# Performance work log

Hardware: AMD Instinct MI355X
Metric: run time of the kernel (lower is better)

The kernel has to match this reference:

```python
import jax, jax.numpy as jnp
import numpy as np

N, IN_DIM, H, ATT_DIM, OUT_DIM = 4096, 512, 8, 64, 64
ATT_BIAS = 0.5


def setup_inputs() -> dict:
    key = jax.random.key(0)
    ks = jax.random.split(key, 12)
    s_in = 1.0 / np.sqrt(IN_DIM)
    s_o = 1.0 / np.sqrt(H * OUT_DIM)
    return {
        "Q": jax.random.normal(ks[0], (N, IN_DIM), jnp.float32),
        "K": jax.random.normal(ks[1], (N, IN_DIM), jnp.float32),
        "V": jax.random.normal(ks[2], (N, IN_DIM), jnp.float32),
        "adj": jax.random.uniform(ks[3], (N, N), jnp.float32),
        "WQ": jax.random.normal(ks[4], (IN_DIM, H * ATT_DIM), jnp.float32) * s_in,
        "bQ": jnp.zeros((H * ATT_DIM,), jnp.float32),
        "WK": jax.random.normal(ks[5], (IN_DIM, H * ATT_DIM), jnp.float32) * s_in,
        "bK": jnp.zeros((H * ATT_DIM,), jnp.float32),
        "WV": jax.random.normal(ks[6], (IN_DIM, H * OUT_DIM), jnp.float32) * s_in,
        "bV": jnp.zeros((H * OUT_DIM,), jnp.float32),
        "WO": jax.random.normal(ks[7], (H * OUT_DIM, OUT_DIM), jnp.float32) * s_o,
        "bO": jnp.zeros((OUT_DIM,), jnp.float32),
    }


def reference(Q, K, V, adj, WQ, bQ, WK, bK, WV, bV, WO, bO):
    scale = ATT_DIM ** -0.5
    q = (Q @ WQ + bQ).reshape(N, H, ATT_DIM)   # [N,H,d]
    k = (K @ WK + bK).reshape(N, H, ATT_DIM)   # [N,H,d]
    v = (V @ WV + bV).reshape(N, H, OUT_DIM)   # [N,H,e]
    # scaled QK^T per head: [H,N,N]
    scores = jnp.einsum("nhd,mhd->hnm", q * scale, k)
    # sigmoid -> bias subtract -> +0.1*adj -> softmax over keys
    scores = jax.nn.sigmoid(scores) - ATT_BIAS + 0.1 * adj[None, :, :]
    attn = jax.nn.softmax(scores, axis=2)
    # attend values (dropout p=0 => identity), concat heads, project
    out = jnp.einsum("hnm,mhe->nhe", attn, v).reshape(N, H * OUT_DIM)
    return out @ WO + bO
```

## Files before the change

kernel.cpp:

```cpp
#include <hip/hip_runtime.h>
#include <hip/hip_bf16.h>

#define N_TOK  4096
#define HD     512
#define NH     8
#define NSPLIT 4
#define QBLK   128
#define NT     ((N_TOK / NSPLIT) / 64)

typedef short v8s __attribute__((ext_vector_type(8)));
typedef float v4f __attribute__((ext_vector_type(4)));
typedef float v16f __attribute__((ext_vector_type(16)));
typedef unsigned short u16;

#define QSCALE   0.18033688011112042f
#define ADJ2     0.14426950408889634f
#define EA0 0.999410f
#define EA1 1.016220f
#define EA2 0.423120f
#define EA3 0.279120f

__device__ __forceinline__ float bf2f(u16 x) {
  union { unsigned int u; float f; } c; c.u = ((unsigned int)x) << 16; return c.f;
}
__device__ __forceinline__ u16 f2bf(float f) {
  union { float f; unsigned int u; } c; c.f = f;
  return (u16)((c.u + 0x7fffu + ((c.u >> 16) & 1u)) >> 16);
}
__device__ __forceinline__ float fast_exp2(float x) {
#if __has_builtin(__builtin_amdgcn_exp2f)
  return __builtin_amdgcn_exp2f(x);
#else
  return exp2f(x);
#endif
}
__device__ __forceinline__ unsigned int pk_bf16(float a, float b) {
  union { __hip_bfloat162 h; unsigned int u; } c;
  c.h = __float22bfloat162_rn(make_float2(a, b));
  return c.u;
}

typedef __attribute__((address_space(1))) const char gchar;
typedef __attribute__((address_space(3))) char lchar;
__device__ __forceinline__ void glds16(const void* g, void* l) {
  __builtin_amdgcn_global_load_lds((gchar*)g, (lchar*)l, 16, 0, 0);
}
__device__ __forceinline__ void plswap(unsigned int& a, unsigned int& b) {
  asm volatile("v_permlane32_swap_b32 %0, %1" : "+v"(a), "+v"(b));
}

__device__ __forceinline__ bool detect_f32(const u16* __restrict__ q) {
  int l = threadIdx.x & 63;
  u16 e = q[2 * l];
  float x = bf2f(e);
  int ex = (e >> 7) & 0xFF;
  float ax = fabsf(x);
  bool ok = (ex != 0xFF) && (ax < 64.f) && (ax > 1e-30f);
  unsigned long long m = __ballot(ok);
  return __popcll(m) < 48;
}
__device__ __forceinline__ float bias_ld(const void* b, int i, bool f32) {
  return f32 ? ((const float*)b)[i] : bf2f(((const u16*)b)[i]);
}

__global__ __launch_bounds__(256) void conv_adjE_k(const void* __restrict__ adj, u16* __restrict__ adjE,
                                                   const u16* __restrict__ Qdet) {
  bool f32 = detect_f32(Qdet);
  int i = blockIdx.x * 256 + threadIdx.x;
  float4 f;
  if (f32) {
    f = ((const float4*)adj)[i];
  } else {
    short4 v = ((const short4*)adj)[i];
    f.x = bf2f((u16)v.x); f.y = bf2f((u16)v.y); f.z = bf2f((u16)v.z); f.w = bf2f((u16)v.w);
  }
  unsigned int d0 = pk_bf16(fast_exp2(f.x * ADJ2), fast_exp2(f.y * ADJ2));
  unsigned int d1 = pk_bf16(fast_exp2(f.z * ADJ2), fast_exp2(f.w * ADJ2));
  ((uint2*)adjE)[i] = make_uint2(d0, d1);
}

__global__ __launch_bounds__(256) void tr_w_k(const void* W0, const void* W1, const void* W2, const void* W3,
                                              u16* t0, u16* t1, u16* t2, u16* t3,
                                              const u16* __restrict__ Qdet) {
  bool f32 = detect_f32(Qdet);
  int z = blockIdx.z;
  const void* in; u16* out; int C;
  if (z == 0)      { in = W0; out = t0; C = 512; }
  else if (z == 1) { in = W1; out = t1; C = 512; }
  else if (z == 2) { in = W2; out = t2; C = 512; }
  else             { in = W3; out = t3; C = 64; if (blockIdx.y) return; }
  const int R = 512;
  __shared__ __align__(16) u16 tile[64][72];
  const int r0 = blockIdx.x * 64, c0 = blockIdx.y * 64;
  const int t = threadIdx.x;
#pragma unroll
  for (int rep = 0; rep < 2; ++rep) {
    int idx = (t + rep * 256) * 8;
    int r = idx >> 6, c = idx & 63;
    if (f32) {
      const float* sp = (const float*)in + (size_t)(r0 + r) * C + (c0 + c);
      float4 a = *(const float4*)sp, b = *(const float4*)(sp + 4);
      uint4 q = make_uint4(pk_bf16(a.x, a.y), pk_bf16(a.z, a.w),
                           pk_bf16(b.x, b.y), pk_bf16(b.z, b.w));
      *(uint4*)&tile[r][c] = q;
    } else {
      *(v8s*)&tile[r][c] = *(const v8s*)((const u16*)in + (size_t)(r0 + r) * C + (c0 + c));
    }
  }
  __syncthreads();
#pragma unroll
  for (int rep = 0; rep < 2; ++rep) {
    int idx = (t + rep * 256) * 8;
    int oc = idx >> 6, orr = idx & 63;
    u16 tmp[8];
#pragma unroll
    for (int j = 0; j < 8; ++j) tmp[j] = tile[orr + j][oc];
    *(v8s*)(out + (size_t)(c0 + oc) * R + (r0 + orr)) = *(v8s*)tmp;
  }
}

__global__ __launch_bounds__(256) void gemm_qkv_k(const void* A0, const void* A1, const void* A2,
                                                  const u16* __restrict__ t0, const u16* __restrict__ t1,
                                                  const u16* __restrict__ t2,
                                                  const void* b0, const void* b1, const void* b2,
                                                  u16* __restrict__ qb, u16* __restrict__ kb,
                                                  u16* __restrict__ vtb) {
  __shared__ __align__(16) u16 As[64][72];
  __shared__ __align__(16) u16 Bs[64][72];
  bool f32 = detect_f32((const u16*)A0);
  int z = blockIdx.z;
  const void* Araw = (z == 0) ? A0 : (z == 1) ? A1 : A2;
  const u16* Bt    = (z == 0) ? t0 : (z == 1) ? t1 : t2;
  const void* bias = (z == 0) ? b0 : (z == 1) ? b1 : b2;
  const bool vt = (z == 2);
  const int i0 = blockIdx.x * 64, j0 = blockIdx.y * 64;
  const int t = threadIdx.x, w = t >> 6, l = t & 63, quad = l >> 4, l15 = l & 15;
  v4f acc[4] = {};
  for (int k0 = 0; k0 < 512; k0 += 64) {
#pragma unroll
    for (int rep = 0; rep < 2; ++rep) {
      int idx = (t + rep * 256) * 8;
      int r = idx >> 6, c = idx & 63;
      if (f32) {
        const float* sp = (const float*)Araw + (size_t)(i0 + r) * 512 + k0 + c;
        float4 fa = *(const float4*)sp, fb = *(const float4*)(sp + 4);
        uint4 q = make_uint4(pk_bf16(fa.x, fa.y), pk_bf16(fa.z, fa.w),
                             pk_bf16(fb.x, fb.y), pk_bf16(fb.z, fb.w));
        *(uint4*)&As[r][c] = q;
      } else {
        *(v8s*)&As[r][c] = *(const v8s*)((const u16*)Araw + (size_t)(i0 + r) * 512 + k0 + c);
      }
      *(v8s*)&Bs[r][c] = *(const v8s*)(Bt + (size_t)(j0 + r) * 512 + k0 + c);
    }
    __syncthreads();
    if (vt) {
#pragma unroll
      for (int h = 0; h < 2; ++h) {
        v8s a = *(const v8s*)&As[w * 16 + l15][h * 32 + quad * 8];
#pragma unroll
        for (int cb = 0; cb < 4; ++cb) {
          v8s b = *(const v8s*)&Bs[cb * 16 + l15][h * 32 + quad * 8];
          acc[cb] = __builtin_amdgcn_mfma_f32_16x16x32_bf16(b, a, acc[cb], 0, 0, 0);
        }
      }
    } else {
#pragma unroll
      for (int h = 0; h < 2; ++h) {
        v8s a = *(const v8s*)&As[w * 16 + l15][h * 32 + quad * 8];
#pragma unroll
        for (int cb = 0; cb < 4; ++cb) {
          v8s b = *(const v8s*)&Bs[cb * 16 + l15][h * 32 + quad * 8];
          acc[cb] = __builtin_amdgcn_mfma_f32_16x16x32_bf16(a, b, acc[cb], 0, 0, 0);
        }
      }
    }
    __syncthreads();
  }
  if (vt) {
#pragma unroll
    for (int cb = 0; cb < 4; ++cb) {
#pragma unroll
      for (int r = 0; r < 4; ++r) {
        int jj = j0 + cb * 16 + quad * 4 + r;
        int ii = i0 + w * 16 + l15;
        vtb[(size_t)jj * N_TOK + ii] = f2bf(acc[cb][r] + bias_ld(bias, jj, f32));
      }
    }
  } else {
    const float oscale = (z == 0) ? QSCALE : 1.0f;
    u16* C = (z == 0) ? qb : kb;
#pragma unroll
    for (int cb = 0; cb < 4; ++cb) {
      int col = j0 + cb * 16 + l15;
      float bv = bias_ld(bias, col, f32);
#pragma unroll
      for (int r = 0; r < 4; ++r) {
        int row = i0 + w * 16 + quad * 4 + r;
        C[(size_t)row * HD + col] = f2bf((acc[cb][r] + bv) * oscale);
      }
    }
  }
}

__global__ __launch_bounds__(256, 4) void attn_kernel(const u16* __restrict__ qb, const u16* __restrict__ kb,
                                                      const u16* __restrict__ vtb, const u16* __restrict__ adjE,
                                                      u16* __restrict__ Opart, float* __restrict__ Lpart) {
  __shared__ __align__(16) u16 Ks[2][64 * 64];
  __shared__ __align__(16) u16 Vs[2][64 * 64];
  const int i0 = blockIdx.x * QBLK, h64 = blockIdx.y * 64, z = blockIdx.z;
  const int t = threadIdx.x, w = t >> 6, l = t & 63;
  const int il = l & 31, h2 = l >> 5, il7 = il & 7;
  const int iRow = i0 + w * 32 + il;

  v8s qf[4];
#pragma unroll
  for (int c = 0; c < 4; ++c)
    qf[c] = *(const v8s*)(qb + (size_t)iRow * HD + h64 + 16 * c + 8 * h2);

  const u16* adjRow = adjE + (size_t)iRow * N_TOK + 4 * h2;

  const int srow = l >> 3;
  const int scol = ((l & 7) ^ srow) * 8;
  const int ldsrow = 16 * w;

  v16f oacc0 = {}, oacc1 = {};
  float lsum = 0.f;
  const int m_begin = z * (N_TOK / NSPLIT);

#pragma unroll
  for (int n = 0; n < 2; ++n) {
    int r = ldsrow + 8 * n + srow;
    glds16(kb + (size_t)(m_begin + r) * HD + h64 + scol, &Ks[0][(ldsrow + 8 * n) * 64]);
    glds16(vtb + (size_t)(h64 + r) * N_TOK + m_begin + scol, &Vs[0][(ldsrow + 8 * n) * 64]);
  }
  __syncthreads();

  int buf = 0;
  for (int mt = 0; mt < NT; ++mt) {
    const int m0 = m_begin + mt * 64;
    if (mt + 1 < NT) {
      const int m1 = m0 + 64;
#pragma unroll
      for (int n = 0; n < 2; ++n) {
        int r = ldsrow + 8 * n + srow;
        glds16(kb + (size_t)(m1 + r) * HD + h64 + scol, &Ks[buf ^ 1][(ldsrow + 8 * n) * 64]);
        glds16(vtb + (size_t)(h64 + r) * N_TOK + m1 + scol, &Vs[buf ^ 1][(ldsrow + 8 * n) * 64]);
      }
    }
    const u16* Kb = &Ks[buf][0];
    const u16* Vb = &Vs[buf][0];

#pragma unroll
    for (int mh = 0; mh < 2; ++mh) {
      uint2 av[4];
#pragma unroll
      for (int rq = 0; rq < 4; ++rq)
        av[rq] = *(const uint2*)(adjRow + m0 + 32 * mh + 8 * rq);

      v16f macc = {};
      __builtin_amdgcn_s_setprio(1);
#pragma unroll
      for (int c = 0; c < 4; ++c) {
        v8s kf = *(const v8s*)(Kb + (32 * mh + il) * 64 + (((2 * c + h2) ^ il7) * 8));
        macc = __builtin_amdgcn_mfma_f32_32x32x16_bf16(kf, qf[c], macc, 0, 0, 0);
      }
      __builtin_amdgcn_s_setprio(0);

      float p[16];
#pragma unroll
      for (int rq = 0; rq < 4; ++rq) {
        union { unsigned int u; float f; } e0, e1, e2, e3;
        e0.u = av[rq].x << 16; e1.u = av[rq].x & 0xFFFF0000u;
        e2.u = av[rq].y << 16; e3.u = av[rq].y & 0xFFFF0000u;
        float r0 = __builtin_amdgcn_rcpf(1.f + fast_exp2(-macc[4 * rq + 0]));
        float r1 = __builtin_amdgcn_rcpf(1.f + fast_exp2(-macc[4 * rq + 1]));
        float r2 = __builtin_amdgcn_rcpf(1.f + fast_exp2(-macc[4 * rq + 2]));
        float r3 = __builtin_amdgcn_rcpf(1.f + fast_exp2(-macc[4 * rq + 3]));
        float p0 = e0.f * fmaf(fmaf(fmaf(EA3, r0, EA2), r0, EA1), r0, EA0);
        float p1 = e1.f * fmaf(fmaf(fmaf(EA3, r1, EA2), r1, EA1), r1, EA0);
        float p2 = e2.f * fmaf(fmaf(fmaf(EA3, r2, EA2), r2, EA1), r2, EA0);
        float p3 = e3.f * fmaf(fmaf(fmaf(EA3, r3, EA2), r3, EA1), r3, EA0);
        lsum += (p0 + p1) + (p2 + p3);
        p[4 * rq + 0] = p0; p[4 * rq + 1] = p1; p[4 * rq + 2] = p2; p[4 * rq + 3] = p3;
      }

      v8s pf[2];
#pragma unroll
      for (int sub = 0; sub < 2; ++sub) {
        unsigned int u0 = pk_bf16(p[8 * sub + 0], p[8 * sub + 1]);
        unsigned int u1 = pk_bf16(p[8 * sub + 2], p[8 * sub + 3]);
        unsigned int u2 = pk_bf16(p[8 * sub + 4], p[8 * sub + 5]);
        unsigned int u3 = pk_bf16(p[8 * sub + 6], p[8 * sub + 7]);
        plswap(u0, u2); plswap(u1, u3);
        union { uint4 q; v8s v; } pu;
        pu.q = make_uint4(u0, u1, u2, u3);
        pf[sub] = pu.v;
      }

      __builtin_amdgcn_s_setprio(1);
#pragma unroll
      for (int sub = 0; sub < 2; ++sub) {
        const int mc = 2 * mh + sub;
        v8s vf0 = *(const v8s*)(Vb + (il) * 64      + (((2 * mc + h2) ^ il7) * 8));
        v8s vf1 = *(const v8s*)(Vb + (32 + il) * 64 + (((2 * mc + h2) ^ il7) * 8));
        oacc0 = __builtin_amdgcn_mfma_f32_32x32x16_bf16(pf[sub], vf0, oacc0, 0, 0, 0);
        oacc1 = __builtin_amdgcn_mfma_f32_32x32x16_bf16(pf[sub], vf1, oacc1, 0, 0, 0);
      }
      __builtin_amdgcn_s_setprio(0);
    }
    __syncthreads();
    buf ^= 1;
  }

  lsum += __shfl_xor(lsum, 32);
  if (l < 32)
    Lpart[((size_t)z * N_TOK + i0 + 32 * w + il) * NH + blockIdx.y] = lsum;

#pragma unroll
  for (int r = 0; r < 16; ++r) {
    int i_local = (r & 3) + 8 * (r >> 2) + 4 * h2;
    size_t row = (size_t)z * N_TOK + i0 + 32 * w + i_local;
    u16* op = Opart + row * HD + h64 + il;
    op[0]  = f2bf(oacc0[r]);
    op[32] = f2bf(oacc1[r]);
  }
}

__global__ __launch_bounds__(256) void gemm_bt(const u16* __restrict__ Opart, const float* __restrict__ Lpart,
                                               const u16* __restrict__ Bt, const void* bias,
                                               void* __restrict__ C, const u16* __restrict__ Qdet) {
  __shared__ __align__(16) u16 As[16][72];
  __shared__ __align__(16) u16 Bs[64][72];
  bool f32 = detect_f32(Qdet);
  const int i0 = blockIdx.x * 16;
  const int t = threadIdx.x, w = t >> 6, l = t & 63, quad = l >> 4, l15 = l & 15;
  v4f acc = {};
  for (int k0 = 0; k0 < 512; k0 += 64) {
    const int h = k0 >> 6;
    if (t < 128) {
      int row = t >> 3, c8 = (t & 7) * 8;
      float lv = 0.f;
#pragma unroll
      for (int s = 0; s < NSPLIT; ++s) lv += Lpart[((size_t)s * N_TOK + i0 + row) * NH + h];
      float rl = __builtin_amdgcn_rcpf(lv);
      float vals[8] = {};
#pragma unroll
      for (int s = 0; s < NSPLIT; ++s) {
        v8s ov = *(const v8s*)(Opart + ((size_t)s * N_TOK + i0 + row) * HD + k0 + c8);
#pragma unroll
        for (int j = 0; j < 8; ++j) vals[j] += bf2f((u16)ov[j]);
      }
      uint4 q = make_uint4(pk_bf16(vals[0] * rl, vals[1] * rl), pk_bf16(vals[2] * rl, vals[3] * rl),
                           pk_bf16(vals[4] * rl, vals[5] * rl), pk_bf16(vals[6] * rl, vals[7] * rl));
      *(uint4*)&As[row][c8] = q;
    }
#pragma unroll
    for (int rep = 0; rep < 2; ++rep) {
      int idx = (t + rep * 256) * 8;
      int r = idx >> 6, c = idx & 63;
      *(v8s*)&Bs[r][c] = *(const v8s*)(Bt + (size_t)r * 512 + k0 + c);
    }
    __syncthreads();
#pragma unroll
    for (int h2 = 0; h2 < 2; ++h2) {
      v8s a = *(const v8s*)&As[l15][h2 * 32 + quad * 8];
      v8s b = *(const v8s*)&Bs[w * 16 + l15][h2 * 32 + quad * 8];
      acc = __builtin_amdgcn_mfma_f32_16x16x32_bf16(a, b, acc, 0, 0, 0);
    }
    __syncthreads();
  }
  {
    int col = w * 16 + l15;
    float bv = bias_ld(bias, col, f32);
#pragma unroll
    for (int r = 0; r < 4; ++r) {
      int row = i0 + quad * 4 + r;
      float v = acc[r] + bv;
      size_t idx = (size_t)row * 64 + col;
      if (f32) ((float*)C)[idx] = v;
      else     ((u16*)C)[idx] = f2bf(v);
    }
  }
}

extern "C" void kernel_launch(void* const* d_in, const int* in_sizes, int n_in,
                              void* d_out, int out_size, void* d_ws, size_t ws_size,
                              hipStream_t stream) {
  (void)in_sizes; (void)n_in; (void)out_size; (void)ws_size;
  const void* Q   = d_in[0];
  const void* K   = d_in[1];
  const void* V   = d_in[2];
  const void* adj = d_in[3];
  const void* WQ  = d_in[4];
  const void* bQ  = d_in[5];
  const void* WK  = d_in[6];
  const void* bK  = d_in[7];
  const void* WV  = d_in[8];
  const void* bV  = d_in[9];
  const void* WO  = d_in[10];
  const void* bO  = d_in[11];
  const u16* Qdet = (const u16*)Q;

  char* p = (char*)d_ws;
  auto alloc = [&](size_t bytes) { char* r = p; p += (bytes + 255) & ~(size_t)255; return r; };
  const size_t SZ = (size_t)N_TOK * HD * 2;

  u16* adjE    = (u16*)alloc((size_t)N_TOK * N_TOK * 2);
  u16* qb      = (u16*)alloc(SZ);
  u16* kb      = (u16*)alloc(SZ);
  u16* vtb     = (u16*)alloc(SZ);
  u16* Opart   = (u16*)alloc((size_t)NSPLIT * SZ);
  float* Lpart = (float*)alloc((size_t)NSPLIT * N_TOK * NH * 4);
  u16* tQ      = (u16*)alloc((size_t)512 * 512 * 2);
  u16* tK      = (u16*)alloc((size_t)512 * 512 * 2);
  u16* tV      = (u16*)alloc((size_t)512 * 512 * 2);
  u16* tO      = (u16*)alloc((size_t)64 * 512 * 2);

  dim3 b256(256);
  conv_adjE_k<<<dim3(16384), b256, 0, stream>>>(adj, adjE, Qdet);
  tr_w_k<<<dim3(8, 8, 4), b256, 0, stream>>>(WQ, WK, WV, WO, tQ, tK, tV, tO, Qdet);
  gemm_qkv_k<<<dim3(64, 8, 3), b256, 0, stream>>>(Q, K, V, tQ, tK, tV,
                                                  bQ, bK, bV, qb, kb, vtb);
  attn_kernel<<<dim3(N_TOK / QBLK, NH, NSPLIT), b256, 0, stream>>>(qb, kb, vtb, adjE, Opart, Lpart);
  gemm_bt<<<dim3(256), b256, 0, stream>>>(Opart, Lpart, tO, bO, d_out, Qdet);
}
```

Before: 262.4 us.

## Quantize precomputed exp(0.1*adj) to uint8 and remap attention grid order

The precomputed exp2(adj*0.1/ln2) factor is stored as an 8-bit fixed-point code over its [1, ~1.105] range instead of bf16, halving the N×N adjacency buffer written by the conversion kernel and read by every attention block. The attention kernel decodes it with a single FMA per element. The launch also becomes a flat 1D grid with a custom mapping from block ID to (query block, head, split), likely meant to improve L2 locality across XCDs. Quantization adds some error to the softmax weights, roughly comparable to bf16 over this narrow range.

Result: slower. 270.1 us (+2.9%).

```diff
diff --git a/kernel.cpp b/kernel.cpp
--- a/kernel.cpp
+++ b/kernel.cpp
@@ -15,6 +15,8 @@
 
 #define QSCALE   0.18033688011112042f
 #define ADJ2     0.14426950408889634f
+#define EC 2424.6f
+#define ER 4.1244e-4f
 #define EA0 0.999410f
 #define EA1 1.016220f
 #define EA2 0.423120f
@@ -63,7 +65,7 @@
   return f32 ? ((const float*)b)[i] : bf2f(((const u16*)b)[i]);
 }
 
-__global__ __launch_bounds__(256) void conv_adjE_k(const void* __restrict__ adj, u16* __restrict__ adjE,
+__global__ __launch_bounds__(256) void conv_adjE_k(const void* __restrict__ adj, unsigned char* __restrict__ adjU8,
                                                    const u16* __restrict__ Qdet) {
   bool f32 = detect_f32(Qdet);
   int i = blockIdx.x * 256 + threadIdx.x;
@@ -74,9 +76,13 @@
     short4 v = ((const short4*)adj)[i];
     f.x = bf2f((u16)v.x); f.y = bf2f((u16)v.y); f.z = bf2f((u16)v.z); f.w = bf2f((u16)v.w);
   }
-  unsigned int d0 = pk_bf16(fast_exp2(f.x * ADJ2), fast_exp2(f.y * ADJ2));
-  unsigned int d1 = pk_bf16(fast_exp2(f.z * ADJ2), fast_exp2(f.w * ADJ2));
-  ((uint2*)adjE)[i] = make_uint2(d0, d1);
+  unsigned e0 = (unsigned)fmaf(fast_exp2(f.x * ADJ2), EC, 0.5f - EC);
+  unsigned e1 = (unsigned)fmaf(fast_exp2(f.y * ADJ2), EC, 0.5f - EC);
+  unsigned e2 = (unsigned)fmaf(fast_exp2(f.z * ADJ2), EC, 0.5f - EC);
+  unsigned e3 = (unsigned)fmaf(fast_exp2(f.w * ADJ2), EC, 0.5f - EC);
+  e0 = e0 > 255u ? 255u : e0; e1 = e1 > 255u ? 255u : e1;
+  e2 = e2 > 255u ? 255u : e2; e3 = e3 > 255u ? 255u : e3;
+  ((unsigned*)adjU8)[i] = e0 | (e1 << 8) | (e2 << 16) | (e3 << 24);
 }
 
 __global__ __launch_bounds__(256) void tr_w_k(const void* W0, const void* W1, const void* W2, const void* W3,
@@ -203,11 +209,17 @@
 }
 
 __global__ __launch_bounds__(256, 4) void attn_kernel(const u16* __restrict__ qb, const u16* __restrict__ kb,
-                                                      const u16* __restrict__ vtb, const u16* __restrict__ adjE,
+                                                      const u16* __restrict__ vtb,
+                                                      const unsigned char* __restrict__ adjU8,
                                                       u16* __restrict__ Opart, float* __restrict__ Lpart) {
   __shared__ __align__(16) u16 Ks[2][64 * 64];
   __shared__ __align__(16) u16 Vs[2][64 * 64];
-  const int i0 = blockIdx.x * QBLK, h64 = blockIdx.y * 64, z = blockIdx.z;
+  const int bid = blockIdx.x;
+  const int g = bid >> 3;
+  const int i0 = ((bid & 7) * 4 + (g & 3)) * QBLK;
+  const int hz = g >> 2;
+  const int hh = hz & 7, z = hz >> 3;
+  const int h64 = hh * 64;
   const int t = threadIdx.x, w = t >> 6, l = t & 63;
   const int il = l & 31, h2 = l >> 5, il7 = il & 7;
   const int iRow = i0 + w * 32 + il;
@@ -217,7 +229,7 @@
   for (int c = 0; c < 4; ++c)
     qf[c] = *(const v8s*)(qb + (size_t)iRow * HD + h64 + 16 * c + 8 * h2);
 
-  const u16* adjRow = adjE + (size_t)iRow * N_TOK + 4 * h2;
+  const unsigned char* adjRow = adjU8 + (size_t)iRow * N_TOK + 4 * h2;
 
   const int srow = l >> 3;
   const int scol = ((l & 7) ^ srow) * 8;
@@ -252,10 +264,10 @@
 
 #pragma unroll
     for (int mh = 0; mh < 2; ++mh) {
-      uint2 av[4];
+      unsigned av[4];
 #pragma unroll
       for (int rq = 0; rq < 4; ++rq)
-        av[rq] = *(const uint2*)(adjRow + m0 + 32 * mh + 8 * rq);
+        av[rq] = *(const unsigned*)(adjRow + m0 + 32 * mh + 8 * rq);
 
       v16f macc = {};
       __builtin_amdgcn_s_setprio(1);
@@ -269,17 +281,19 @@
       float p[16];
 #pragma unroll
       for (int rq = 0; rq < 4; ++rq) {
-        union { unsigned int u; float f; } e0, e1, e2, e3;
-        e0.u = av[rq].x << 16; e1.u = av[rq].x & 0xFFFF0000u;
-        e2.u = av[rq].y << 16; e3.u = av[rq].y & 0xFFFF0000u;
+        unsigned ac = av[rq];
+        float E0 = fmaf((float)(ac & 0xFFu),         ER, 1.0f);
+        float E1 = fmaf((float)((ac >> 8) & 0xFFu),  ER, 1.0f);
+        float E2 = fmaf((float)((ac >> 16) & 0xFFu), ER, 1.0f);
+        float E3 = fmaf((float)(ac >> 24),           ER, 1.0f);
         float r0 = __builtin_amdgcn_rcpf(1.f + fast_exp2(-macc[4 * rq + 0]));
         float r1 = __builtin_amdgcn_rcpf(1.f + fast_exp2(-macc[4 * rq + 1]));
         float r2 = __builtin_amdgcn_rcpf(1.f + fast_exp2(-macc[4 * rq + 2]));
         float r3 = __builtin_amdgcn_rcpf(1.f + fast_exp2(-macc[4 * rq + 3]));
-        float p0 = e0.f * fmaf(fmaf(fmaf(EA3, r0, EA2), r0, EA1), r0, EA0);
-        float p1 = e1.f * fmaf(fmaf(fmaf(EA3, r1, EA2), r1, EA1), r1, EA0);
-        float p2 = e2.f * fmaf(fmaf(fmaf(EA3, r2, EA2), r2, EA1), r2, EA0);
-        float p3 = e3.f * fmaf(fmaf(fmaf(EA3, r3, EA2), r3, EA1), r3, EA0);
+        float p0 = E0 * fmaf(fmaf(fmaf(EA3, r0, EA2), r0, EA1), r0, EA0);
+        float p1 = E1 * fmaf(fmaf(fmaf(EA3, r1, EA2), r1, EA1), r1, EA0);
+        float p2 = E2 * fmaf(fmaf(fmaf(EA3, r2, EA2), r2, EA1), r2, EA0);
+        float p3 = E3 * fmaf(fmaf(fmaf(EA3, r3, EA2), r3, EA1), r3, EA0);
         lsum += (p0 + p1) + (p2 + p3);
         p[4 * rq + 0] = p0; p[4 * rq + 1] = p1; p[4 * rq + 2] = p2; p[4 * rq + 3] = p3;
       }
@@ -314,7 +328,7 @@
 
   lsum += __shfl_xor(lsum, 32);
   if (l < 32)
-    Lpart[((size_t)z * N_TOK + i0 + 32 * w + il) * NH + blockIdx.y] = lsum;
+    Lpart[((size_t)z * N_TOK + i0 + 32 * w + il) * NH + hh] = lsum;
 
 #pragma unroll
   for (int r = 0; r < 16; ++r) {
@@ -405,7 +419,7 @@
   auto alloc = [&](size_t bytes) { char* r = p; p += (bytes + 255) & ~(size_t)255; return r; };
   const size_t SZ = (size_t)N_TOK * HD * 2;
 
-  u16* adjE    = (u16*)alloc((size_t)N_TOK * N_TOK * 2);
+  unsigned char* adjU8 = (unsigned char*)alloc((size_t)N_TOK * N_TOK);
   u16* qb      = (u16*)alloc(SZ);
   u16* kb      = (u16*)alloc(SZ);
   u16* vtb     = (u16*)alloc(SZ);
@@ -417,10 +431,10 @@
   u16* tO      = (u16*)alloc((size_t)64 * 512 * 2);
 
   dim3 b256(256);
-  conv_adjE_k<<<dim3(16384), b256, 0, stream>>>(adj, adjE, Qdet);
+  conv_adjE_k<<<dim3(16384), b256, 0, stream>>>(adj, adjU8, Qdet);
   tr_w_k<<<dim3(8, 8, 4), b256, 0, stream>>>(WQ, WK, WV, WO, tQ, tK, tV, tO, Qdet);
   gemm_qkv_k<<<dim3(64, 8, 3), b256, 0, stream>>>(Q, K, V, tQ, tK, tV,
                                                   bQ, bK, bV, qb, kb, vtb);
-  attn_kernel<<<dim3(N_TOK / QBLK, NH, NSPLIT), b256, 0, stream>>>(qb, kb, vtb, adjE, Opart, Lpart);
+  attn_kernel<<<dim3(1024), b256, 0, stream>>>(qb, kb, vtb, adjU8, Opart, Lpart);
   gemm_bt<<<dim3(256), b256, 0, stream>>>(Opart, Lpart, tO, bO, d_out, Qdet);
 }
```
